# Performance work log

Measured on AMD Instinct MI355X. Metric: run time of the kernel, lower is better.

Reference implementation:

```python
import jax, jax.numpy as jnp
import numpy as np

LN_EPS = 1e-6


def setup_inputs() -> dict:
    key = jax.random.key(0)
    ks = jax.random.split(key, 8)
    B, L, D = 8, 4096, 1024
    s = 1.0 / np.sqrt(D)
    inputs = jax.random.normal(ks[0], (B, L, D), dtype=jnp.float32)
    # PositionwiseFeedForward params (d_ff == d_model here)
    w1 = jax.random.normal(ks[1], (D, D), dtype=jnp.float32) * s
    b1 = jnp.zeros((D,), dtype=jnp.float32)
    w2 = jax.random.normal(ks[2], (D, D), dtype=jnp.float32) * s
    b2 = jnp.zeros((D,), dtype=jnp.float32)
    ln_g = jnp.ones((D,), dtype=jnp.float32)
    ln_b = jnp.zeros((D,), dtype=jnp.float32)
    # gating layer: Linear(2D, 2D)
    wg = jax.random.normal(ks[3], (2 * D, 2 * D), dtype=jnp.float32) * (1.0 / np.sqrt(2 * D))
    bg = jnp.zeros((2 * D,), dtype=jnp.float32)
    return {"inputs": inputs, "w1": w1, "b1": b1, "w2": w2, "b2": b2,
            "ln_g": ln_g, "ln_b": ln_b, "wg": wg, "bg": bg}


def _layer_norm(x, g, b):
    mu = jnp.mean(x, axis=-1, keepdims=True)
    var = jnp.mean(jnp.square(x - mu), axis=-1, keepdims=True)
    return (x - mu) * jax.lax.rsqrt(var + LN_EPS) * g + b


def reference(inputs, w1, b1, w2, b2, ln_g, ln_b, wg, bg):
    B, L, D = inputs.shape
    # Cumulative average: identical math to tril(ones)/arange mask @ inputs,
    # computed in O(L) via prefix sum instead of an O(L^2) matmul.
    denom = jnp.arange(1, L + 1, dtype=inputs.dtype)[:, None]  # [L,1]
    avg = jnp.cumsum(inputs, axis=1) / denom                    # [B,L,D]
    # PositionwiseFeedForward (eval mode, dropout=0): LN -> relu(Linear) -> Linear -> +residual
    h = _layer_norm(avg, ln_g, ln_b)
    inter = jax.nn.relu(jnp.einsum('bld,df->blf', h, w1) + b1)
    avg_out = jnp.einsum('blf,fd->bld', inter, w2) + b2 + avg
    # Gating: Linear on concat(inputs, avg_out), split, sigmoid gates
    concat = jnp.concatenate([inputs, avg_out], axis=-1)        # [B,L,2D]
    gates = jnp.einsum('ble,ef->blf', concat, wg) + bg          # [B,L,2D]
    input_gate, forget_gate = gates[..., :D], gates[..., D:]
    out = jax.nn.sigmoid(input_gate) * inputs + jax.nn.sigmoid(forget_gate) * avg_out
    return out
```

## Files before the change

### kernel.cpp

```cpp
#include <hip/hip_runtime.h>

typedef __bf16 bf16_t;
typedef bf16_t bf16x8 __attribute__((ext_vector_type(8)));
typedef bf16_t bf16x4 __attribute__((ext_vector_type(4)));
typedef float  f32x4  __attribute__((ext_vector_type(4)));

typedef const __attribute__((address_space(1))) void* gptr_t;
typedef __attribute__((address_space(3))) void* sptr_t;

#define BATCH 8
#define SEQL  4096
#define DIM   1024
#define MROWS 32768

__device__ __forceinline__ float sigmoidf_(float v) {
    return 1.0f / (1.0f + __expf(-v));
}

template <int PERM>
__global__ void transpose_cast(const float* __restrict__ W, bf16_t* __restrict__ WT,
                               int K, int N) {
    __shared__ float s[32][33];
    int tx = threadIdx.x, ty = threadIdx.y;
    int x = blockIdx.x * 32 + tx;
    int y = blockIdx.y * 32 + ty;
    s[ty][tx] = W[(size_t)y * N + x];
    __syncthreads();
    int n = blockIdx.x * 32 + ty;
    int k = blockIdx.y * 32 + tx;
    int nd = n;
    if (PERM) {
        if (n < 1024) nd = ((n >> 6) << 7) + (n & 63);
        else          nd = (((n - 1024) >> 6) << 7) + 64 + ((n - 1024) & 63);
    }
    WT[(size_t)nd * K + k] = (bf16_t)s[tx][ty];
}

__global__ void scan_chunks(const float* __restrict__ x, float* __restrict__ cs) {
    int tid = threadIdx.x;
    int b = blockIdx.x >> 6, c = blockIdx.x & 63;
    const f32x4* x4 = (const f32x4*)x;
    size_t base = ((size_t)b * SEQL + (size_t)c * 64) * 256 + tid;
    f32x4 s0 = {0.f, 0.f, 0.f, 0.f}, s1 = {0.f, 0.f, 0.f, 0.f};
#pragma unroll 8
    for (int j = 0; j < 64; j += 2) {
        s0 += x4[base + (size_t)j * 256];
        s1 += x4[base + (size_t)(j + 1) * 256];
    }
    ((f32x4*)cs)[((size_t)(b << 6) + c) * 256 + tid] = s0 + s1;
}

__global__ void scan_prefix(float* __restrict__ cs) {
    int t = blockIdx.x * 256 + threadIdx.x;
    int b = t >> 10, d = t & 1023;
    size_t base = (size_t)(b << 6) * 1024 + d;
    float v[64];
#pragma unroll
    for (int c = 0; c < 64; ++c) v[c] = cs[base + (size_t)c * 1024];
    float run = 0.f;
#pragma unroll
    for (int c = 0; c < 64; ++c) {
        float tv = v[c];
        cs[base + (size_t)c * 1024] = run;
        run += tv;
    }
}

__global__ __launch_bounds__(256) void scan_ln(
    const float* __restrict__ x, const float* __restrict__ cs,
    const float* __restrict__ g, const float* __restrict__ bb,
    float* __restrict__ avg, bf16_t* __restrict__ hb, bf16_t* __restrict__ xb) {
    int tid = threadIdx.x;
    int wave = tid >> 6, lane = tid & 63;
    int b = blockIdx.x >> 6, c = blockIdx.x & 63;
    __shared__ float red[8];
    const f32x4* x4 = (const f32x4*)x;
    f32x4* avg4 = (f32x4*)avg;
    bf16x4* hb4 = (bf16x4*)hb;
    bf16x4* xb4 = (bf16x4*)xb;
    f32x4 run = ((const f32x4*)cs)[((size_t)(b << 6) + c) * 256 + tid];
    f32x4 gv = ((const f32x4*)g)[tid];
    f32x4 bv = ((const f32x4*)bb)[tid];
    size_t row0 = (size_t)b * SEQL + (size_t)c * 64;
    f32x4 xv = x4[row0 * 256 + tid];
    for (int j = 0; j < 64; ++j) {
        size_t ridx = (row0 + j) * 256 + tid;
        f32x4 xnext = {0.f, 0.f, 0.f, 0.f};
        if (j < 63) xnext = x4[ridx + 256];
        run += xv;
        float inv = 1.0f / (float)(c * 64 + j + 1);
        f32x4 av = run * inv;
        avg4[ridx] = av;
        bf16x4 xo = { (bf16_t)xv[0], (bf16_t)xv[1], (bf16_t)xv[2], (bf16_t)xv[3] };
        xb4[ridx] = xo;
        float s  = av[0] + av[1] + av[2] + av[3];
        float sq = av[0]*av[0] + av[1]*av[1] + av[2]*av[2] + av[3]*av[3];
#pragma unroll
        for (int off = 32; off; off >>= 1) {
            s  += __shfl_xor(s, off);
            sq += __shfl_xor(sq, off);
        }
        if (lane == 0) { red[wave] = s; red[4 + wave] = sq; }
        __syncthreads();
        s  = red[0] + red[1] + red[2] + red[3];
        sq = red[4] + red[5] + red[6] + red[7];
        float mu  = s * (1.f / DIM);
        float var = sq * (1.f / DIM) - mu * mu;
        var = var < 0.f ? 0.f : var;
        float rs = 1.0f / sqrtf(var + 1e-6f);
        f32x4 hn = (av - mu) * rs * gv + bv;
        bf16x4 ho = { (bf16_t)hn[0], (bf16_t)hn[1], (bf16_t)hn[2], (bf16_t)hn[3] };
        hb4[ridx] = ho;
        __syncthreads();
        xv = xnext;
    }
}

template <int EPI>
__global__ __launch_bounds__(512, 2) void gemm_bt(
    const bf16_t* __restrict__ A0, const bf16_t* __restrict__ A1, int kSplit,
    const bf16_t* __restrict__ Bt, int N, int K,
    const float* __restrict__ bias, const float* __restrict__ addsrc,
    const float* __restrict__ xsrc,
    float* __restrict__ outf, bf16_t* __restrict__ outb) {
    __shared__ char smem[131072];
    const int tid = threadIdx.x;
    const int wave = tid >> 6, lane = tid & 63;

    const int nwg = gridDim.x;
    const int q8 = nwg >> 3;
    const int lid = (blockIdx.x & 7) * q8 + ((int)blockIdx.x >> 3);
    const int nBlocks = N >> 8;
    const int m0 = (lid / nBlocks) << 8;
    const int n0 = (lid % nBlocks) << 8;

    const int wm = (wave >> 2) << 7;
    const int wn = (wave & 3) << 6;
    const int lrow16 = lane & 15;
    const int ksw0 = ((((lane >> 4) + 0) ^ (lane & 7)) << 3);
    const int ksw1 = ((((lane >> 4) + 4) ^ (lane & 7)) << 3);

    f32x4 acc[8][4] = {};

    const int nT = K >> 6;

    auto STAGE = [&](int k0, int buf) {
        const bf16_t* Asrc;
        int ak0;
        if (k0 < kSplit) { Asrc = A0; ak0 = k0; }
        else             { Asrc = A1; ak0 = k0 - kSplit; }
        bf16_t* As = (bf16_t*)(smem + buf * 65536);
        bf16_t* Bs = As + 256 * 64;
#pragma unroll
        for (int rd = 0; rd < 4; ++rd) {
            int ci = tid + (rd << 9);
            int row = ci >> 3, ch = ci & 7;
            int chs = ch ^ (row & 7);
            const bf16_t* gp = Asrc + (size_t)(m0 + row) * kSplit + ak0 + (chs << 3);
            bf16_t* sb = As + (size_t)(ci & ~63) * 8;
            __builtin_amdgcn_global_load_lds((gptr_t)gp, (sptr_t)sb, 16, 0, 0);
        }
#pragma unroll
        for (int rd = 0; rd < 4; ++rd) {
            int ci = tid + (rd << 9);
            int row = ci >> 3, ch = ci & 7;
            int chs = ch ^ (row & 7);
            const bf16_t* gp = Bt + (size_t)(n0 + row) * K + k0 + (chs << 3);
            bf16_t* sb = Bs + (size_t)(ci & ~63) * 8;
            __builtin_amdgcn_global_load_lds((gptr_t)gp, (sptr_t)sb, 16, 0, 0);
        }
    };

    STAGE(0, 0);

    for (int t = 0; t < nT; ++t) {
        const int p = t & 1;
        __builtin_amdgcn_s_barrier();
        if (t + 1 < nT) {
            STAGE((t + 1) << 6, p ^ 1);
            asm volatile("s_waitcnt vmcnt(8)" ::: "memory");
        } else {
            asm volatile("s_waitcnt vmcnt(0)" ::: "memory");
        }
        __builtin_amdgcn_s_barrier();
        __builtin_amdgcn_sched_barrier(0);
        const bf16_t* As = (const bf16_t*)(smem + p * 65536);
        const bf16_t* Bs = As + 256 * 64;
        bf16x8 bfv[4];
#pragma unroll
        for (int ph = 0; ph < 4; ++ph) {
            const int kk = ph >> 1, mh = ph & 1;
            const int ksw = kk ? ksw1 : ksw0;
            if (mh == 0) {
#pragma unroll
                for (int ni = 0; ni < 4; ++ni)
                    bfv[ni] = *(const bf16x8*)&Bs[(wn + ni * 16 + lrow16) * 64 + ksw];
            }
            bf16x8 af[4];
#pragma unroll
            for (int mi = 0; mi < 4; ++mi)
                af[mi] = *(const bf16x8*)&As[(wm + (mh * 4 + mi) * 16 + lrow16) * 64 + ksw];
            __builtin_amdgcn_s_setprio(1);
#pragma unroll
            for (int mi = 0; mi < 4; ++mi)
#pragma unroll
                for (int ni = 0; ni < 4; ++ni)
                    acc[mh * 4 + mi][ni] = __builtin_amdgcn_mfma_f32_16x16x32_bf16(
                        af[mi], bfv[ni], acc[mh * 4 + mi][ni], 0, 0, 0);
            __builtin_amdgcn_s_setprio(0);
        }
    }

    const int erow = (lane >> 4) << 2;

    if (EPI == 4) {
        __syncthreads();
        float* xch = (float*)smem;
        const int T = (n0 + wn) >> 7;
        const int pairOff = ((((wave >> 2) << 1) | ((wave >> 1) & 1))) << 13;
        if (wn & 64) {
#pragma unroll
            for (int mi = 0; mi < 8; ++mi) {
#pragma unroll
                for (int ni = 0; ni < 4; ++ni) {
                    int dc = ni * 16 + lrow16;
                    float bcol = bias[1024 + T * 64 + dc];
                    int d = T * 64 + dc;
#pragma unroll
                    for (int r = 0; r < 4; ++r) {
                        int rowW = mi * 16 + erow + r;
                        int row = m0 + wm + rowW;
                        float v = acc[mi][ni][r] + bcol;
                        int sw = ((rowW >> 2) & 1) << 4;
                        xch[pairOff + rowW * 64 + (dc ^ sw)] =
                            sigmoidf_(v) * addsrc[(size_t)row * 1024 + d];
                    }
                }
            }
        }
        __syncthreads();
        if (!(wn & 64)) {
#pragma unroll
            for (int mi = 0; mi < 8; ++mi) {
#pragma unroll
                for (int ni = 0; ni < 4; ++ni) {
                    int dc = ni * 16 + lrow16;
                    float bcol = bias[T * 64 + dc];
                    int d = T * 64 + dc;
#pragma unroll
                    for (int r = 0; r < 4; ++r) {
                        int rowW = mi * 16 + erow + r;
                        int row = m0 + wm + rowW;
                        float v = acc[mi][ni][r] + bcol;
                        int sw = ((rowW >> 2) & 1) << 4;
                        float tot = sigmoidf_(v) * xsrc[(size_t)row * 1024 + d]
                                  + xch[pairOff + rowW * 64 + (dc ^ sw)];
                        outf[(size_t)row * 1024 + d] = tot;
                    }
                }
            }
        }
        return;
    }

#pragma unroll
    for (int mi = 0; mi < 8; ++mi) {
#pragma unroll
        for (int ni = 0; ni < 4; ++ni) {
            int col = n0 + wn + ni * 16 + lrow16;
            float bcol = bias[col];
#pragma unroll
            for (int r = 0; r < 4; ++r) {
                int row = m0 + wm + mi * 16 + erow + r;
                size_t idx = (size_t)row * N + col;
                float v = acc[mi][ni][r];
                if (EPI == 1) {
                    v += bcol;
                    v = v > 0.f ? v : 0.f;
                    outb[idx] = (bf16_t)v;
                } else {
                    v += bcol + addsrc[idx];
                    outf[idx] = v;
                    outb[idx] = (bf16_t)v;
                }
            }
        }
    }
}

extern "C" void kernel_launch(void* const* d_in, const int* in_sizes, int n_in,
                              void* d_out, int out_size, void* d_ws, size_t ws_size,
                              hipStream_t stream) {
    const float* inp  = (const float*)d_in[0];
    const float* w1   = (const float*)d_in[1];
    const float* b1   = (const float*)d_in[2];
    const float* w2   = (const float*)d_in[3];
    const float* b2   = (const float*)d_in[4];
    const float* ln_g = (const float*)d_in[5];
    const float* ln_b = (const float*)d_in[6];
    const float* wg   = (const float*)d_in[7];
    const float* bg   = (const float*)d_in[8];
    float* out = (float*)d_out;

    char* w = (char*)d_ws;
    float*  avg    = (float*)w;   w += (size_t)MROWS * DIM * 4;
    float*  avgout = (float*)w;   w += (size_t)MROWS * DIM * 4;
    bf16_t* xb     = (bf16_t*)w;  w += (size_t)MROWS * DIM * 2;
    bf16_t* hb     = (bf16_t*)w;  w += (size_t)MROWS * DIM * 2;
    bf16_t* interb = (bf16_t*)w;  w += (size_t)MROWS * DIM * 2;
    bf16_t* w1t    = (bf16_t*)w;  w += (size_t)DIM * DIM * 2;
    bf16_t* w2t    = (bf16_t*)w;  w += (size_t)DIM * DIM * 2;
    bf16_t* wgt    = (bf16_t*)w;  w += (size_t)2 * DIM * 2 * DIM * 2;
    float*  csum   = (float*)w;   w += (size_t)BATCH * 64 * DIM * 4;
    bf16_t* aob    = hb;

    transpose_cast<0><<<dim3(32, 32), dim3(32, 32), 0, stream>>>(w1, w1t, DIM, DIM);
    transpose_cast<0><<<dim3(32, 32), dim3(32, 32), 0, stream>>>(w2, w2t, DIM, DIM);
    transpose_cast<1><<<dim3(64, 64), dim3(32, 32), 0, stream>>>(wg, wgt, 2 * DIM, 2 * DIM);

    scan_chunks<<<BATCH * 64, 256, 0, stream>>>(inp, csum);
    scan_prefix<<<32, 256, 0, stream>>>(csum);
    scan_ln<<<BATCH * 64, 256, 0, stream>>>(inp, csum, ln_g, ln_b, avg, hb, xb);

    gemm_bt<1><<<(MROWS / 256) * (DIM / 256), 512, 0, stream>>>(
        hb, hb, DIM, w1t, DIM, DIM, b1, nullptr, nullptr, nullptr, interb);

    gemm_bt<2><<<(MROWS / 256) * (DIM / 256), 512, 0, stream>>>(
        interb, interb, DIM, w2t, DIM, DIM, b2, avg, nullptr, avgout, aob);

    gemm_bt<4><<<(MROWS / 256) * (2 * DIM / 256), 512, 0, stream>>>(
        xb, aob, DIM, wgt, 2 * DIM, 2 * DIM, bg, avgout, inp, out, nullptr);
}
```

Baseline: 942.4 us.

## Interleave fine-grained A/B tile staging with MFMA phases in GEMM main loop

Replaces the double-buffered loop, which staged a whole K tile and then computed it, with an 8-phase loop over two K tiles per iteration. Each phase issues a quarter of the next tile's global-to-LDS loads, waits with a partial vmcnt, and runs 16 MFMAs. B fragments are kept in registers across the two M halves, so they are read from LDS only once. The aim is to overlap memory traffic with matrix math more evenly and cut stall time at barriers. The cost is more barriers per tile, and the final iteration prefetches tiles past the end of K, which reads out-of-range addresses.

After: 878.6 us. 1.07x faster.

```diff
diff --git a/kernel.cpp b/kernel.cpp
--- a/kernel.cpp
+++ b/kernel.cpp
@@ -142,74 +142,121 @@
 
     f32x4 acc[8][4] = {};
 
-    const int nT = K >> 6;
-
-    auto STAGE = [&](int k0, int buf) {
-        const bf16_t* Asrc;
-        int ak0;
+    auto stageA = [&](int kt, int buf, int mh) {
+        const int k0 = kt << 6;
+        const bf16_t* Asrc; int ak0;
         if (k0 < kSplit) { Asrc = A0; ak0 = k0; }
         else             { Asrc = A1; ak0 = k0 - kSplit; }
-        bf16_t* As = (bf16_t*)(smem + buf * 65536);
-        bf16_t* Bs = As + 256 * 64;
-#pragma unroll
-        for (int rd = 0; rd < 4; ++rd) {
-            int ci = tid + (rd << 9);
+#pragma unroll
+        for (int rr = 0; rr < 2; ++rr) {
+            int ci = tid + ((mh + rr * 2) << 9);
             int row = ci >> 3, ch = ci & 7;
             int chs = ch ^ (row & 7);
             const bf16_t* gp = Asrc + (size_t)(m0 + row) * kSplit + ak0 + (chs << 3);
-            bf16_t* sb = As + (size_t)(ci & ~63) * 8;
+            bf16_t* sb = (bf16_t*)(smem + (buf << 16)) + (size_t)(ci & ~63) * 8;
             __builtin_amdgcn_global_load_lds((gptr_t)gp, (sptr_t)sb, 16, 0, 0);
         }
-#pragma unroll
-        for (int rd = 0; rd < 4; ++rd) {
-            int ci = tid + (rd << 9);
+    };
+    auto stageB = [&](int kt, int buf, int half) {
+        const int k0 = kt << 6;
+#pragma unroll
+        for (int rr = 0; rr < 2; ++rr) {
+            int ci = tid + ((half * 2 + rr) << 9);
             int row = ci >> 3, ch = ci & 7;
             int chs = ch ^ (row & 7);
             const bf16_t* gp = Bt + (size_t)(n0 + row) * K + k0 + (chs << 3);
-            bf16_t* sb = Bs + (size_t)(ci & ~63) * 8;
+            bf16_t* sb = (bf16_t*)(smem + (buf << 16) + 32768) + (size_t)(ci & ~63) * 8;
             __builtin_amdgcn_global_load_lds((gptr_t)gp, (sptr_t)sb, 16, 0, 0);
         }
     };
 
-    STAGE(0, 0);
-
-    for (int t = 0; t < nT; ++t) {
-        const int p = t & 1;
-        __builtin_amdgcn_s_barrier();
-        if (t + 1 < nT) {
-            STAGE((t + 1) << 6, p ^ 1);
-            asm volatile("s_waitcnt vmcnt(8)" ::: "memory");
-        } else {
-            asm volatile("s_waitcnt vmcnt(0)" ::: "memory");
-        }
-        __builtin_amdgcn_s_barrier();
-        __builtin_amdgcn_sched_barrier(0);
-        const bf16_t* As = (const bf16_t*)(smem + p * 65536);
-        const bf16_t* Bs = As + 256 * 64;
-        bf16x8 bfv[4];
-#pragma unroll
-        for (int ph = 0; ph < 4; ++ph) {
-            const int kk = ph >> 1, mh = ph & 1;
-            const int ksw = kk ? ksw1 : ksw0;
-            if (mh == 0) {
-#pragma unroll
-                for (int ni = 0; ni < 4; ++ni)
-                    bfv[ni] = *(const bf16x8*)&Bs[(wn + ni * 16 + lrow16) * 64 + ksw];
-            }
-            bf16x8 af[4];
-#pragma unroll
-            for (int mi = 0; mi < 4; ++mi)
-                af[mi] = *(const bf16x8*)&As[(wm + (mh * 4 + mi) * 16 + lrow16) * 64 + ksw];
-            __builtin_amdgcn_s_setprio(1);
-#pragma unroll
-            for (int mi = 0; mi < 4; ++mi)
-#pragma unroll
-                for (int ni = 0; ni < 4; ++ni)
-                    acc[mh * 4 + mi][ni] = __builtin_amdgcn_mfma_f32_16x16x32_bf16(
-                        af[mi], bfv[ni], acc[mh * 4 + mi][ni], 0, 0, 0);
-            __builtin_amdgcn_s_setprio(0);
-        }
-    }
+    bf16x8 af[4], bfv0[4], bfv1[4];
+    auto readsAB = [&](int buf, int mh, int ksw, bf16x8* bfv) {
+        const bf16_t* As_ = (const bf16_t*)(smem + (buf << 16));
+        const bf16_t* Bs_ = As_ + 16384;
+#pragma unroll
+        for (int ni = 0; ni < 4; ++ni)
+            bfv[ni] = *(const bf16x8*)&Bs_[(wn + ni * 16 + lrow16) * 64 + ksw];
+#pragma unroll
+        for (int mi = 0; mi < 4; ++mi)
+            af[mi] = *(const bf16x8*)&As_[(wm + (mh * 4 + mi) * 16 + lrow16) * 64 + ksw];
+    };
+    auto readsA = [&](int buf, int mh, int ksw) {
+        const bf16_t* As_ = (const bf16_t*)(smem + (buf << 16));
+#pragma unroll
+        for (int mi = 0; mi < 4; ++mi)
+            af[mi] = *(const bf16x8*)&As_[(wm + (mh * 4 + mi) * 16 + lrow16) * 64 + ksw];
+    };
+    auto mfma16 = [&](int mh, bf16x8* bfv) {
+        __builtin_amdgcn_s_setprio(1);
+#pragma unroll
+        for (int mi = 0; mi < 4; ++mi)
+#pragma unroll
+            for (int ni = 0; ni < 4; ++ni)
+                acc[mh * 4 + mi][ni] = __builtin_amdgcn_mfma_f32_16x16x32_bf16(
+                    af[mi], bfv[ni], acc[mh * 4 + mi][ni], 0, 0, 0);
+        __builtin_amdgcn_s_setprio(0);
+    };
+
+#define BAR_  __builtin_amdgcn_s_barrier()
+#define SB_   __builtin_amdgcn_sched_barrier(0)
+#define VMW6_ asm volatile("s_waitcnt vmcnt(6)" ::: "memory")
+
+    stageA(0, 0, 0);
+    stageB(0, 0, 0);
+    stageB(0, 0, 1);
+    stageA(1, 1, 0);
+    stageA(0, 0, 1);
+
+    const int nIter = K >> 7;
+#pragma nounroll
+    for (int i = 0; i < nIter; ++i) {
+        const int t2 = i << 1;
+        stageB(t2 + 1, 1, 0);
+        VMW6_; BAR_; SB_;
+        readsAB(0, 0, ksw0, bfv0); mfma16(0, bfv0);
+        SB_; BAR_; SB_;
+
+        stageB(t2 + 1, 1, 1);
+        BAR_; SB_;
+        readsAB(0, 0, ksw1, bfv1); mfma16(0, bfv1);
+        SB_; BAR_; SB_;
+
+        stageA(t2 + 2, 0, 0);
+        VMW6_; BAR_; SB_;
+        readsA(0, 1, ksw0); mfma16(1, bfv0);
+        SB_; BAR_; SB_;
+
+        stageA(t2 + 1, 1, 1);
+        BAR_; SB_;
+        readsA(0, 1, ksw1); mfma16(1, bfv1);
+        SB_; BAR_; SB_;
+
+        stageB(t2 + 2, 0, 0);
+        VMW6_; BAR_; SB_;
+        readsAB(1, 0, ksw0, bfv0); mfma16(0, bfv0);
+        SB_; BAR_; SB_;
+
+        stageB(t2 + 2, 0, 1);
+        BAR_; SB_;
+        readsAB(1, 0, ksw1, bfv1); mfma16(0, bfv1);
+        SB_; BAR_; SB_;
+
+        stageA(t2 + 3, 1, 0);
+        VMW6_; BAR_; SB_;
+        readsA(1, 1, ksw0); mfma16(1, bfv0);
+        SB_; BAR_; SB_;
+
+        stageA(t2 + 2, 0, 1);
+        BAR_; SB_;
+        readsA(1, 1, ksw1); mfma16(1, bfv1);
+        SB_; BAR_; SB_;
+    }
+    asm volatile("s_waitcnt vmcnt(0)" ::: "memory");
+
+#undef BAR_
+#undef SB_
+#undef VMW6_
 
     const int erow = (lane >> 4) << 2;
 
```

## Restructure GEMM to 256x128 tiles with triple-buffered K=32 pipeline

Applied to the files above, without the earlier changes.

The bf16 GEMM moves from 512-thread 256x256 tiles with a double-buffered K=64 loop to 256-thread 256x128 tiles with a triple-buffered K=32 loop. A and B loads are staged separately and interleaved with the two MFMA halves. The aim is lower LDS use (72KB instead of 128KB) so more blocks fit per CU, plus better overlap of global loads with compute. In exchange there are more barriers per unit of work, and each block does less B-tile reuse. The gating epilogue's LDS exchange layout is adapted to the new wave arrangement.

Result: no change. 927.2 us (-1.6%).

```diff
diff --git a/kernel.cpp b/kernel.cpp
--- a/kernel.cpp
+++ b/kernel.cpp
@@ -117,108 +117,123 @@
 }
 
 template <int EPI>
-__global__ __launch_bounds__(512, 2) void gemm_bt(
+__global__ __launch_bounds__(256, 2) void gemm_bt(
     const bf16_t* __restrict__ A0, const bf16_t* __restrict__ A1, int kSplit,
     const bf16_t* __restrict__ Bt, int N, int K,
     const float* __restrict__ bias, const float* __restrict__ addsrc,
     const float* __restrict__ xsrc,
     float* __restrict__ outf, bf16_t* __restrict__ outb) {
-    __shared__ char smem[131072];
+    __shared__ char smem[73728];
     const int tid = threadIdx.x;
     const int wave = tid >> 6, lane = tid & 63;
 
     const int nwg = gridDim.x;
     const int q8 = nwg >> 3;
     const int lid = (blockIdx.x & 7) * q8 + ((int)blockIdx.x >> 3);
-    const int nBlocks = N >> 8;
+    const int nBlocks = N >> 7;
     const int m0 = (lid / nBlocks) << 8;
-    const int n0 = (lid % nBlocks) << 8;
-
-    const int wm = (wave >> 2) << 7;
-    const int wn = (wave & 3) << 6;
+    const int n0 = (lid % nBlocks) << 7;
+    const int wm = (wave >> 1) << 7;
+    const int wn = (wave & 1) << 6;
     const int lrow16 = lane & 15;
-    const int ksw0 = ((((lane >> 4) + 0) ^ (lane & 7)) << 3);
-    const int ksw1 = ((((lane >> 4) + 4) ^ (lane & 7)) << 3);
+    const int ksw = (((lane >> 4) ^ ((lane >> 1) & 3)) << 3);
 
     f32x4 acc[8][4] = {};
 
-    const int nT = K >> 6;
-
-    auto STAGE = [&](int k0, int buf) {
-        const bf16_t* Asrc;
-        int ak0;
+    auto stageA = [&](int kt, int buf) {
+        int k0 = kt << 5;
+        if (k0 > K - 32) k0 = K - 32;
+        const bf16_t* Asrc; int ak0;
         if (k0 < kSplit) { Asrc = A0; ak0 = k0; }
         else             { Asrc = A1; ak0 = k0 - kSplit; }
-        bf16_t* As = (bf16_t*)(smem + buf * 65536);
-        bf16_t* Bs = As + 256 * 64;
+        char* base = smem + buf * 24576;
 #pragma unroll
         for (int rd = 0; rd < 4; ++rd) {
-            int ci = tid + (rd << 9);
-            int row = ci >> 3, ch = ci & 7;
-            int chs = ch ^ (row & 7);
+            int ci = tid + (rd << 8);
+            int row = ci >> 2, ch = ci & 3;
+            int chs = ch ^ ((row >> 1) & 3);
             const bf16_t* gp = Asrc + (size_t)(m0 + row) * kSplit + ak0 + (chs << 3);
-            bf16_t* sb = As + (size_t)(ci & ~63) * 8;
+            bf16_t* sb = (bf16_t*)base + (size_t)(ci & ~63) * 8;
             __builtin_amdgcn_global_load_lds((gptr_t)gp, (sptr_t)sb, 16, 0, 0);
         }
-#pragma unroll
-        for (int rd = 0; rd < 4; ++rd) {
-            int ci = tid + (rd << 9);
-            int row = ci >> 3, ch = ci & 7;
-            int chs = ch ^ (row & 7);
+    };
+    auto stageB = [&](int kt, int buf) {
+        int k0 = kt << 5;
+        if (k0 > K - 32) k0 = K - 32;
+        char* base = smem + buf * 24576 + 16384;
+#pragma unroll
+        for (int rd = 0; rd < 2; ++rd) {
+            int ci = tid + (rd << 8);
+            int row = ci >> 2, ch = ci & 3;
+            int chs = ch ^ ((row >> 1) & 3);
             const bf16_t* gp = Bt + (size_t)(n0 + row) * K + k0 + (chs << 3);
-            bf16_t* sb = Bs + (size_t)(ci & ~63) * 8;
+            bf16_t* sb = (bf16_t*)base + (size_t)(ci & ~63) * 8;
             __builtin_amdgcn_global_load_lds((gptr_t)gp, (sptr_t)sb, 16, 0, 0);
         }
     };
 
-    STAGE(0, 0);
-
+    bf16x8 af[4], bfv[4];
+    auto readA4 = [&](int buf, int half) {
+        const bf16_t* As_ = (const bf16_t*)(smem + buf * 24576);
+#pragma unroll
+        for (int mi = 0; mi < 4; ++mi)
+            af[mi] = *(const bf16x8*)&As_[(wm + (half * 4 + mi) * 16 + lrow16) * 32 + ksw];
+    };
+    auto readB4 = [&](int buf) {
+        const bf16_t* Bs_ = (const bf16_t*)(smem + buf * 24576 + 16384);
+#pragma unroll
+        for (int ni = 0; ni < 4; ++ni)
+            bfv[ni] = *(const bf16x8*)&Bs_[(wn + ni * 16 + lrow16) * 32 + ksw];
+    };
+    auto mfma16 = [&](int half) {
+        __builtin_amdgcn_s_setprio(1);
+#pragma unroll
+        for (int mi = 0; mi < 4; ++mi)
+#pragma unroll
+            for (int ni = 0; ni < 4; ++ni)
+                acc[half * 4 + mi][ni] = __builtin_amdgcn_mfma_f32_16x16x32_bf16(
+                    af[mi], bfv[ni], acc[half * 4 + mi][ni], 0, 0, 0);
+        __builtin_amdgcn_s_setprio(0);
+    };
+
+#define BAR_  __builtin_amdgcn_s_barrier()
+#define SB_   __builtin_amdgcn_sched_barrier(0)
+#define LG0_  asm volatile("s_waitcnt lgkmcnt(0)" ::: "memory")
+#define VMW6_ asm volatile("s_waitcnt vmcnt(6)" ::: "memory")
+
+    stageA(0, 0); stageB(0, 0);
+    stageA(1, 1); stageB(1, 1);
+    VMW6_;
+    BAR_;
+
+    const int nT = K >> 5;
+    int cb = 0, st = 2;
+#pragma nounroll
     for (int t = 0; t < nT; ++t) {
-        const int p = t & 1;
-        __builtin_amdgcn_s_barrier();
-        if (t + 1 < nT) {
-            STAGE((t + 1) << 6, p ^ 1);
-            asm volatile("s_waitcnt vmcnt(8)" ::: "memory");
-        } else {
-            asm volatile("s_waitcnt vmcnt(0)" ::: "memory");
-        }
-        __builtin_amdgcn_s_barrier();
-        __builtin_amdgcn_sched_barrier(0);
-        const bf16_t* As = (const bf16_t*)(smem + p * 65536);
-        const bf16_t* Bs = As + 256 * 64;
-        bf16x8 bfv[4];
-#pragma unroll
-        for (int ph = 0; ph < 4; ++ph) {
-            const int kk = ph >> 1, mh = ph & 1;
-            const int ksw = kk ? ksw1 : ksw0;
-            if (mh == 0) {
-#pragma unroll
-                for (int ni = 0; ni < 4; ++ni)
-                    bfv[ni] = *(const bf16x8*)&Bs[(wn + ni * 16 + lrow16) * 64 + ksw];
-            }
-            bf16x8 af[4];
-#pragma unroll
-            for (int mi = 0; mi < 4; ++mi)
-                af[mi] = *(const bf16x8*)&As[(wm + (mh * 4 + mi) * 16 + lrow16) * 64 + ksw];
-            __builtin_amdgcn_s_setprio(1);
-#pragma unroll
-            for (int mi = 0; mi < 4; ++mi)
-#pragma unroll
-                for (int ni = 0; ni < 4; ++ni)
-                    acc[mh * 4 + mi][ni] = __builtin_amdgcn_mfma_f32_16x16x32_bf16(
-                        af[mi], bfv[ni], acc[mh * 4 + mi][ni], 0, 0, 0);
-            __builtin_amdgcn_s_setprio(0);
-        }
-    }
+        readB4(cb); readA4(cb, 0);
+        stageA(t + 2, st);
+        BAR_; LG0_; SB_; mfma16(0); BAR_;
+        readA4(cb, 1);
+        stageB(t + 2, st);
+        VMW6_;
+        BAR_; LG0_; SB_; mfma16(1); BAR_;
+        cb = (cb == 2) ? 0 : cb + 1;
+        st = (st == 2) ? 0 : st + 1;
+    }
+    asm volatile("s_waitcnt vmcnt(0)" ::: "memory");
+
+#undef BAR_
+#undef SB_
+#undef LG0_
+#undef VMW6_
 
     const int erow = (lane >> 4) << 2;
 
     if (EPI == 4) {
         __syncthreads();
         float* xch = (float*)smem;
-        const int T = (n0 + wn) >> 7;
-        const int pairOff = ((((wave >> 2) << 1) | ((wave >> 1) & 1))) << 13;
-        if (wn & 64) {
+        const int T = n0 >> 7;
+        if (wn) {
 #pragma unroll
             for (int mi = 0; mi < 8; ++mi) {
 #pragma unroll
@@ -232,14 +247,14 @@
                         int row = m0 + wm + rowW;
                         float v = acc[mi][ni][r] + bcol;
                         int sw = ((rowW >> 2) & 1) << 4;
-                        xch[pairOff + rowW * 64 + (dc ^ sw)] =
+                        xch[(wm + rowW) * 64 + (dc ^ sw)] =
                             sigmoidf_(v) * addsrc[(size_t)row * 1024 + d];
                     }
                 }
             }
         }
         __syncthreads();
-        if (!(wn & 64)) {
+        if (!wn) {
 #pragma unroll
             for (int mi = 0; mi < 8; ++mi) {
 #pragma unroll
@@ -254,7 +269,7 @@
                         float v = acc[mi][ni][r] + bcol;
                         int sw = ((rowW >> 2) & 1) << 4;
                         float tot = sigmoidf_(v) * xsrc[(size_t)row * 1024 + d]
-                                  + xch[pairOff + rowW * 64 + (dc ^ sw)];
+                                  + xch[(wm + rowW) * 64 + (dc ^ sw)];
                         outf[(size_t)row * 1024 + d] = tot;
                     }
                 }
@@ -322,12 +337,12 @@
     scan_prefix<<<32, 256, 0, stream>>>(csum);
     scan_ln<<<BATCH * 64, 256, 0, stream>>>(inp, csum, ln_g, ln_b, avg, hb, xb);
 
-    gemm_bt<1><<<(MROWS / 256) * (DIM / 256), 512, 0, stream>>>(
+    gemm_bt<1><<<(MROWS / 256) * (DIM / 128), 256, 0, stream>>>(
         hb, hb, DIM, w1t, DIM, DIM, b1, nullptr, nullptr, nullptr, interb);
 
-    gemm_bt<2><<<(MROWS / 256) * (DIM / 256), 512, 0, stream>>>(
+    gemm_bt<2><<<(MROWS / 256) * (DIM / 128), 256, 0, stream>>>(
         interb, interb, DIM, w2t, DIM, DIM, b2, avg, nullptr, avgout, aob);
 
-    gemm_bt<4><<<(MROWS / 256) * (2 * DIM / 256), 512, 0, stream>>>(
+    gemm_bt<4><<<(MROWS / 256) * (2 * DIM / 128), 256, 0, stream>>>(
         xb, aob, DIM, wgt, 2 * DIM, 2 * DIM, bg, avgout, inp, out, nullptr);
 }
```
